# Optimization experiments

Measured on AMD Instinct MI355X. Metric: run time of the kernel, lower is better.

## Reference

```python
import jax, jax.numpy as jnp
import numpy as np

T_STEPS = 4000          # T_ms / dt = 1000 / 0.25
N_IN, N_OUT = 64, 10
HID = [1024, 1024]
DT, TAU = 0.25, 10.0
BETA = float(np.exp(-DT / TAU))   # beta_snn
THR = 1.0                          # thr_snn
SLOPE = 1.0                        # spike_snn uses slope=1.0
W_STD = 32.0                       # W_STD_CUBA

@jax.custom_vjp
def spike(u):
    # SurrogateSpike.forward: heaviside on (mem - thr)
    return (u >= 0).astype(u.dtype)

def _spike_fwd(u):
    return spike(u), u

def _spike_bwd(u, g):
    # fast-sigmoid surrogate: slope / (1 + slope*|u|)^2
    grad = SLOPE / (1.0 + SLOPE * jnp.abs(u)) ** 2
    return (g * grad,)

spike.defvjp(_spike_fwd, _spike_bwd)

def setup_inputs() -> dict:
    key = jax.random.key(0)
    ks = jax.random.split(key, 8)
    B = 16
    # Bernoulli(0.05) input spike train, time-major [T, B, N_IN]
    input_spikes = (jax.random.uniform(ks[0], (T_STEPS, B, N_IN)) < 0.05).astype(jnp.float32)
    sizes = [N_IN] + HID + [N_OUT]
    inp = {"input_spikes": input_spikes}
    for i, (n_pre, n_post) in enumerate(zip(sizes[:-1], sizes[1:])):
        # init_weight 'normal': clamp(N(0, W_STD), min=0) / n_pre
        w = jnp.maximum(jax.random.normal(ks[i + 1], (n_pre, n_post)) * W_STD, 0.0) / n_pre
        inp[f"W{i}"] = w.astype(jnp.float32)
        inp[f"b{i}"] = jnp.zeros((n_post,), jnp.float32)
    return inp

def reference(input_spikes, W0, b0, W1, b1, W2, b2):
    # Dale's law: feedforward weights clamped >= 0 in forward
    Ws = [jnp.maximum(W, 0.0) for W in (W0, W1, W2)]
    bs = [b0, b1, b2]
    B = input_spikes.shape[1]
    sizes = HID + [N_OUT]
    mems0 = tuple(jnp.zeros((B, n), input_spikes.dtype) for n in sizes)

    def step(mems, s_in):
        s = s_in
        new_mems = []
        for l in range(len(Ws)):
            I = s @ Ws[l] + bs[l]                 # [B, n_post]
            m = BETA * mems[l] + I                # LIF decay + drive
            sp = spike(m - THR)                   # surrogate-grad spike
            m = jnp.where(sp > 0, 0.0, m)         # hard reset to zero
            new_mems.append(m)
            s = sp
        return tuple(new_mems), s                 # emit output-layer spikes

    _, out_spikes = jax.lax.scan(step, mems0, input_spikes)
    return out_spikes  # [T, B, N_OUT]
```

## Files before the change

kernel.cpp:

```cpp
#include <hip/hip_runtime.h>
#include <hip/hip_bf16.h>
#include <math.h>


#define T_STEPS 4000
#define NB 16
#define N_IN 64
#define NH 1024
#define N_OUT 10
#define SEGO 40
#define SEGH 40

typedef __attribute__((ext_vector_type(8))) short bf16x8;
typedef __attribute__((ext_vector_type(4))) float f32x4;
typedef __hip_bfloat16 bf16;
typedef unsigned long long u64;

#define ASG(p) (const __attribute__((address_space(1))) void*)(p)
#define ASL(p) (__attribute__((address_space(3))) void*)(p)


__global__ __launch_bounds__(256) void k_prep(
    const float* __restrict__ in_sp, u64* __restrict__ mask,
    const float* __restrict__ W1, bf16* __restrict__ BT1,
    const float* __restrict__ W2, bf16* __restrict__ BT2,
    float* __restrict__ mst, int nM, int ZB, int MB) {
    __shared__ float Wlds[64][65];
    int b = blockIdx.x;
    const int tid = threadIdx.x;
    if (b < ZB) {
        int i = b * 256 + tid;
        if (i < nM) mst[i] = 0.f;
        return;
    }
    b -= ZB;
    if (b < MB) {
        int w = b * 4 + (tid >> 6);
        int lane = tid & 63;
        float v = in_sp[(size_t)w * 64 + lane];
        u64 bal = __ballot(v > 0.5f);
        if (lane == 0) mask[w] = bal;
        return;
    }
    b -= MB;
    if (b < 256) {
        const int lane = tid & 63;
        const int wr   = tid >> 6;
        const int k0 = (b & 15) * 64;
        const int n0 = (b >> 4) * 64;
#pragma unroll
        for (int rr = 0; rr < 16; ++rr) {
            int kl = wr * 16 + rr;
            Wlds[kl][lane] = W1[(size_t)(k0 + kl) * 1024 + n0 + lane];
        }
        __syncthreads();
#pragma unroll
        for (int rr = 0; rr < 16; ++rr) {
            int nl = wr * 16 + rr;
            float w = fmaxf(Wlds[lane][nl], 0.f);
            bf16 h = __float2bfloat16(w);
            float hf = __bfloat162float(h);
            bf16 l = __float2bfloat16(w - hf);
            size_t base = (size_t)(n0 + nl) * 2048 + 2 * k0 + lane;
            BT1[base] = h;
            BT1[base + 64] = l;
        }
        return;
    }
    b -= 256;
    {
        int idx = b * 256 + tid;
        int total = 128 * 2 * NH;
        if (idx >= total) return;
        int n  = idx / (2 * NH);
        int k2 = idx - n * (2 * NH);
        int lo = (k2 >= NH);
        int k = lo ? (k2 - NH) : k2;
        float v = 0.f;
        if (n < N_OUT) {
            float w = fmaxf(W2[(size_t)k * N_OUT + n], 0.f);
            float hi = __bfloat162float(__float2bfloat16(w));
            v = lo ? (w - hi) : w;
        }
        BT2[idx] = __float2bfloat16(v);
    }
}

__global__ void k_unpack(const u64* __restrict__ BITS, float* __restrict__ out,
                         int total) {
    int idx = blockIdx.x * 256 + threadIdx.x;
    if (idx >= total) return;
    int t   = idx / (NB * N_OUT);
    int rem = idx - t * (NB * N_OUT);
    int b = rem / N_OUT;
    int k = rem - b * N_OUT;
    u64 w = BITS[(size_t)(t / SEGO) * 256 + b * 16 + k];
    out[idx] = ((w >> (t % SEGO)) & 1ULL) ? 1.f : 0.f;
}


__device__ __forceinline__ void scan_out_body(
    const float* __restrict__ I2, const float* __restrict__ bias,
    float* __restrict__ mstate, u64* __restrict__ BITS,
    int Tc, float* seg, int tid) {
    float* segA = seg;
    float* segB = seg + SEGO * 256;
    const bool act = tid < 256;
    const int lane = tid & 63;
    const int wave = tid >> 6;
    const int k = tid & 15;
    float m = 0.f, bj = 0.f;
    if (act) {
        m = mstate[tid];
        bj = (k < N_OUT) ? bias[k] : 0.f;
    }
    const int nseg = Tc / SEGO;

#define O_PREFETCH(SEGBUF, SIDX)                                            \
    if (act) {                                                              \
        const float* src = I2 + (size_t)(SIDX) * SEGO * 256                 \
                              + (size_t)wave * 256 + lane * 4;              \
        _Pragma("unroll")                                                   \
        for (int g = 0; g < SEGO / 4; ++g)                                  \
            __builtin_amdgcn_global_load_lds(                               \
                ASG(src + (size_t)(g * 4) * 256),                           \
                ASL(&SEGBUF[(g * 4 + wave) * 256]), 16, 0, 0);              \
    }

#define O_PROC(SEGBUF, SIDX)                                                \
    if (act) {                                                              \
        u64 obits = 0;                                                      \
        _Pragma("unroll")                                                   \
        for (int sb = 0; sb < SEGO / 8; ++sb) {                             \
            float v[8];                                                     \
            _Pragma("unroll")                                               \
            for (int u = 0; u < 8; ++u)                                     \
                v[u] = SEGBUF[(sb * 8 + u) * 256 + tid];                    \
            _Pragma("unroll")                                               \
            for (int u = 0; u < 8; ++u) {                                   \
                m = fmaf(beta_c, m, v[u] + bj);                             \
                bool sp = (m >= 1.0f);                                      \
                obits |= ((u64)(sp ? 1 : 0)) << (sb * 8 + u);               \
                m = sp ? 0.f : m;                                           \
            }                                                               \
        }                                                                   \
        BITS[(size_t)(SIDX) * 256 + tid] = obits;                           \
    }

    const float beta_c = 0.97530991202833261687f;
    O_PREFETCH(segA, 0);
    O_PREFETCH(segB, 1);
    asm volatile("s_waitcnt vmcnt(10)" ::: "memory");
    __builtin_amdgcn_sched_barrier(0);
    __builtin_amdgcn_s_barrier();
    for (int s = 0; s < nseg; s += 2) {
        O_PROC(segA, s);
        if (s + 2 < nseg) {
            O_PREFETCH(segA, s + 2);
            asm volatile("s_waitcnt vmcnt(11)" ::: "memory");
        } else {
            asm volatile("s_waitcnt vmcnt(1)" ::: "memory");
        }
        __builtin_amdgcn_sched_barrier(0);
        __builtin_amdgcn_s_barrier();
        O_PROC(segB, s + 1);
        if (s + 3 < nseg) {
            O_PREFETCH(segB, s + 3);
            asm volatile("s_waitcnt vmcnt(11)" ::: "memory");
            __builtin_amdgcn_sched_barrier(0);
            __builtin_amdgcn_s_barrier();
        } else if (s + 2 < nseg) {
            asm volatile("s_waitcnt vmcnt(1)" ::: "memory");
            __builtin_amdgcn_sched_barrier(0);
            __builtin_amdgcn_s_barrier();
        }
    }
    if (act) mstate[tid] = m;
#undef O_PREFETCH
#undef O_PROC
}

__global__ __launch_bounds__(256) void k_scan_out(
    const float* __restrict__ I2, const float* __restrict__ bias,
    float* __restrict__ mstate, u64* __restrict__ BITS, int Tc) {
    __shared__ __align__(16) float seg[2 * SEGO * 256];
    scan_out_body(I2, bias, mstate, BITS, Tc, seg, threadIdx.x);
}


__global__ __launch_bounds__(256) void k_gemm_thin(
    const bf16* __restrict__ A, const bf16* __restrict__ BT,
    float* __restrict__ C) {
    const int tid  = threadIdx.x;
    const int lane = tid & 63;
    const int wave = tid >> 6;
    const int r16 = lane & 15;
    const int kg  = lane >> 4;
    const int m0 = blockIdx.x * 64 + wave * 16;
    f32x4 acc = {};
    const bf16* ap = A + (size_t)(m0 + r16) * 1024 + kg * 8;
    const bf16* bh = BT + (size_t)r16 * 2048 + kg * 8;
    const bf16* bl = bh + 1024;
#pragma unroll 8
    for (int kt = 0; kt < 32; ++kt) {
        const int ka = kt * 32;
        bf16x8 af  = *(const bf16x8*)(ap + ka);
        bf16x8 bfh = *(const bf16x8*)(bh + ka);
        bf16x8 bfl = *(const bf16x8*)(bl + ka);
        acc = __builtin_amdgcn_mfma_f32_16x16x32_bf16(af, bfh, acc, 0, 0, 0);
        acc = __builtin_amdgcn_mfma_f32_16x16x32_bf16(af, bfl, acc, 0, 0, 0);
    }
#pragma unroll
    for (int rr = 0; rr < 4; ++rr)
        C[(size_t)(m0 + kg * 4 + rr) * 16 + r16] = acc[rr];
}


__global__ __launch_bounds__(512) void k_gemm8(
    const bf16* __restrict__ A, const bf16* __restrict__ BT,
    float* __restrict__ C, int gx,
    const float* __restrict__ I2t, const float* __restrict__ b2t,
    float* __restrict__ m2t, u64* __restrict__ BITSt, int tcT, int doTail) {
    __shared__ __align__(16) char LDS[131072];
    const int tid  = threadIdx.x;

    if (doTail && (int)blockIdx.x == (int)gridDim.x - 1) {
        scan_out_body(I2t, b2t, m2t, BITSt, tcT, (float*)LDS, tid);
        return;
    }

    const int KA = 1024;
    const int nwg = gridDim.x - doTail;
    const int wg  = blockIdx.x;
    const int q = nwg >> 3, r = nwg & 7;
    const int xcd = wg & 7, idx0 = wg >> 3;
    const int swz = (xcd < r ? xcd * (q + 1) : r * (q + 1) + (xcd - r) * q) + idx0;
    const int gy = nwg / gx;
    const int n0 = (swz % gy) * 256;
    const int m0 = (swz / gy) * 256;

    const int lane = tid & 63;
    const int wave = tid >> 6;
    const int wm = (wave >> 2) * 128;
    const int wn = (wave & 3) * 64;
    const int r16l = lane & 15;
    const int kg   = lane >> 4;
    const int hA   = wave >> 2;
    const int hB   = (wave & 3) >> 1;
    const int wn64 = wave & 1;

    const int po = (r16l * 64 + kg * 16) ^ (((r16l >> 3) & 1) << 5);
    const char* bA[2] = { LDS + hA * 16384 + po,
                          LDS + 32768 + hA * 16384 + po };
    const char* bB[2] = { LDS + 65536 + hB * 16384 + po,
                          LDS + 98304 + hB * 16384 + po };
    const int bOff = wn64 * 8192;

    int s_row[2], s_col[2];
#pragma unroll
    for (int rr = 0; rr < 2; ++rr) {
        int d = (rr * 512 + tid) * 16;
        int l = d ^ (((d >> 9) & 1) << 5);
        int sub = l >> 10;
        int w = l & 1023;
        s_row[rr] = (sub >> 1) * 16 + (w >> 6);
        s_col[rr] = ((sub & 1) * 64 + (w & 63)) >> 1;
    }

#define STAGE_A(ADST, HALF, K0)                                             \
    {                                                                       \
        _Pragma("unroll")                                                   \
        for (int rr = 0; rr < 2; ++rr)                                      \
            __builtin_amdgcn_global_load_lds(                               \
                ASG(A + (size_t)(m0 + (HALF) * 128 + s_row[rr]) * KA        \
                    + (K0) + s_col[rr]),                                    \
                ASL(LDS + (ADST) * 32768 + (HALF) * 16384                   \
                    + (rr * 512 + wave * 64) * 16),                         \
                16, 0, 0);                                                  \
    }
#define STAGE_B(BUF, HALF, K0)                                              \
    {                                                                       \
        _Pragma("unroll")                                                   \
        for (int rr = 0; rr < 2; ++rr)                                      \
            __builtin_amdgcn_global_load_lds(                               \
                ASG(BT + (size_t)(n0 + (HALF) * 128 + s_row[rr]) * 2048     \
                    + (K0) + s_col[rr]),                                    \
                ASL(LDS + 65536 + (BUF) * 32768 + (HALF) * 16384            \
                    + (rr * 512 + wave * 64) * 16),                         \
                16, 0, 0);                                                  \
    }

    f32x4 acc[8][4] = {};
    bf16x8 a[4][2], b[4][2];

#define MM(MIB, NIB)                                                        \
    {                                                                       \
        _Pragma("unroll")                                                   \
        for (int i = 0; i < 4; ++i)                                         \
            _Pragma("unroll")                                               \
            for (int j = 0; j < 2; ++j) {                                   \
                acc[(MIB) + i][(NIB) + j] =                                 \
                    __builtin_amdgcn_mfma_f32_16x16x32_bf16(                \
                        a[i][0], b[(NIB) + j][0], acc[(MIB) + i][(NIB) + j], 0, 0, 0); \
                acc[(MIB) + i][(NIB) + j] =                                 \
                    __builtin_amdgcn_mfma_f32_16x16x32_bf16(                \
                        a[i][1], b[(NIB) + j][1], acc[(MIB) + i][(NIB) + j], 0, 0, 0); \
            }                                                               \
    }

#define PH_SYNC()                                                           \
    __builtin_amdgcn_s_barrier();                                           \
    asm volatile("s_waitcnt lgkmcnt(0)" ::: "memory");                      \
    __builtin_amdgcn_sched_barrier(0);

#define KT_EVEN(ABUF, BKN, AKN)                                             \
    {                                                                       \
        _Pragma("unroll")                                                   \
        for (int i = 0; i < 4; ++i) {                                       \
            a[i][0] = *(const bf16x8*)(bA[ABUF] + i * 2048);                \
            a[i][1] = *(const bf16x8*)(bA[ABUF] + i * 2048 + 1024);         \
        }                                                                   \
        _Pragma("unroll")                                                   \
        for (int j = 0; j < 2; ++j) {                                       \
            b[j][0] = *(const bf16x8*)(bB[0] + bOff + j * 2048);            \
            b[j][1] = *(const bf16x8*)(bB[0] + bOff + j * 2048 + 1024);     \
        }                                                                   \
        PH_SYNC();                                                          \
        __builtin_amdgcn_s_setprio(1);                                      \
        MM(0, 0);                                                           \
        __builtin_amdgcn_s_setprio(0);                                      \
        __builtin_amdgcn_s_barrier();                                       \
        _Pragma("unroll")                                                   \
        for (int j = 0; j < 2; ++j) {                                       \
            b[2 + j][0] = *(const bf16x8*)(bB[0] + bOff + (2 + j) * 2048);  \
            b[2 + j][1] = *(const bf16x8*)(bB[0] + bOff + (2 + j) * 2048 + 1024); \
        }                                                                   \
        PH_SYNC();                                                          \
        __builtin_amdgcn_s_setprio(1);                                      \
        MM(0, 2);                                                           \
        __builtin_amdgcn_s_setprio(0);                                      \
        __builtin_amdgcn_s_barrier();                                       \
        _Pragma("unroll")                                                   \
        for (int i = 0; i < 4; ++i) {                                       \
            a[i][0] = *(const bf16x8*)(bA[ABUF] + (4 + i) * 2048);          \
            a[i][1] = *(const bf16x8*)(bA[ABUF] + (4 + i) * 2048 + 1024);   \
        }                                                                   \
        STAGE_B(0, 0, BKN);                                                 \
        STAGE_B(0, 1, BKN);                                                 \
        PH_SYNC();                                                          \
        __builtin_amdgcn_s_setprio(1);                                      \
        MM(4, 0);                                                           \
        __builtin_amdgcn_s_setprio(0);                                      \
        __builtin_amdgcn_s_barrier();                                       \
        STAGE_A((ABUF) ^ 1, 0, AKN);                                        \
        STAGE_A((ABUF) ^ 1, 1, AKN);                                        \
        PH_SYNC();                                                          \
        __builtin_amdgcn_s_setprio(1);                                      \
        MM(4, 2);                                                           \
        __builtin_amdgcn_s_setprio(0);                                      \
        asm volatile("s_waitcnt vmcnt(8)" ::: "memory");                    \
        __builtin_amdgcn_sched_barrier(0);                                  \
        __builtin_amdgcn_s_barrier();                                       \
    }

#define KT_ODD(ABUF, BKN)                                                   \
    {                                                                       \
        _Pragma("unroll")                                                   \
        for (int i = 0; i < 4; ++i) {                                       \
            a[i][0] = *(const bf16x8*)(bA[ABUF] + i * 2048);                \
            a[i][1] = *(const bf16x8*)(bA[ABUF] + i * 2048 + 1024);         \
        }                                                                   \
        _Pragma("unroll")                                                   \
        for (int j = 0; j < 2; ++j) {                                       \
            b[j][0] = *(const bf16x8*)(bB[1] + bOff + j * 2048);            \
            b[j][1] = *(const bf16x8*)(bB[1] + bOff + j * 2048 + 1024);     \
        }                                                                   \
        PH_SYNC();                                                          \
        __builtin_amdgcn_s_setprio(1);                                      \
        MM(0, 0);                                                           \
        __builtin_amdgcn_s_setprio(0);                                      \
        __builtin_amdgcn_s_barrier();                                       \
        _Pragma("unroll")                                                   \
        for (int j = 0; j < 2; ++j) {                                       \
            b[2 + j][0] = *(const bf16x8*)(bB[1] + bOff + (2 + j) * 2048);  \
            b[2 + j][1] = *(const bf16x8*)(bB[1] + bOff + (2 + j) * 2048 + 1024); \
        }                                                                   \
        PH_SYNC();                                                          \
        __builtin_amdgcn_s_setprio(1);                                      \
        MM(0, 2);                                                           \
        __builtin_amdgcn_s_setprio(0);                                      \
        __builtin_amdgcn_s_barrier();                                       \
        _Pragma("unroll")                                                   \
        for (int i = 0; i < 4; ++i) {                                       \
            a[i][0] = *(const bf16x8*)(bA[ABUF] + (4 + i) * 2048);          \
            a[i][1] = *(const bf16x8*)(bA[ABUF] + (4 + i) * 2048 + 1024);   \
        }                                                                   \
        STAGE_B(1, 0, BKN);                                                 \
        STAGE_B(1, 1, BKN);                                                 \
        PH_SYNC();                                                          \
        __builtin_amdgcn_s_setprio(1);                                      \
        MM(4, 0);                                                           \
        __builtin_amdgcn_s_setprio(0);                                      \
        __builtin_amdgcn_s_barrier();                                       \
        PH_SYNC();                                                          \
        __builtin_amdgcn_s_setprio(1);                                      \
        MM(4, 2);                                                           \
        __builtin_amdgcn_s_setprio(0);                                      \
        asm volatile("s_waitcnt vmcnt(4)" ::: "memory");                    \
        __builtin_amdgcn_sched_barrier(0);                                  \
        __builtin_amdgcn_s_barrier();                                       \
    }

    STAGE_B(0, 0, 0);  STAGE_B(0, 1, 0);
    STAGE_A(0, 0, 0);  STAGE_A(0, 1, 0);
    STAGE_B(1, 0, 64); STAGE_B(1, 1, 64);
    asm volatile("s_waitcnt vmcnt(4)" ::: "memory");
    __builtin_amdgcn_sched_barrier(0);
    __builtin_amdgcn_s_barrier();

    for (int it2 = 0; it2 < 16; it2 += 2) {
        const int ak1 = (64 * (it2 + 1)) & 1023;
        const int be1 = (128 * (it2 + 1)) & 2047;
        KT_EVEN(0, be1, ak1);
        KT_ODD(0, be1 + 64);
        const int ak2 = (64 * (it2 + 2)) & 1023;
        const int be2 = (128 * (it2 + 2)) & 2047;
        KT_EVEN(1, be2, ak2);
        KT_ODD(1, be2 + 64);
    }
    asm volatile("s_waitcnt vmcnt(0)" ::: "memory");
    __builtin_amdgcn_sched_barrier(0);

#pragma unroll
    for (int mi = 0; mi < 8; ++mi)
#pragma unroll
        for (int ni = 0; ni < 4; ++ni)
#pragma unroll
            for (int rr = 0; rr < 4; ++rr) {
                int row = m0 + wm + mi * 16 + kg * 4 + rr;
                int col = n0 + wn + ni * 16 + r16l;
                C[(size_t)row * 1024 + col] = acc[mi][ni][rr];
            }
#undef KT_ODD
#undef KT_EVEN
#undef PH_SYNC
#undef MM
#undef STAGE_A
#undef STAGE_B
}


__global__ __launch_bounds__(64) void k_scan_l0(
    const u64* __restrict__ mask,
    const float* __restrict__ W0,
    const float* __restrict__ bias,
    float* __restrict__ mstate, bf16* __restrict__ S, int Tc, float beta) {
    __shared__ float Ilds[2][16][68];
    const int lane = threadIdx.x;
    const int gid  = blockIdx.x * 64 + lane;
    const int b  = blockIdx.x >> 4;
    const int q  = blockIdx.x & 15;
    const int j0 = q * 64;
    const int r16 = lane & 15;
    const int kg  = lane >> 4;
    bf16x8 bh[4][2], bl[4][2];
#pragma unroll
    for (int jt = 0; jt < 4; ++jt)
#pragma unroll
        for (int kk = 0; kk < 2; ++kk)
#pragma unroll
            for (int e = 0; e < 8; ++e) {
                int k = kk * 32 + kg * 8 + e;
                float w = fmaxf(W0[(size_t)k * 1024 + j0 + jt * 16 + r16], 0.f);
                bf16 h = __float2bfloat16(w);
                float hf = __bfloat162float(h);
                bf16 l = __float2bfloat16(w - hf);
                bh[jt][kk][e] = *(short*)&h;
                bl[jt][kk][e] = *(short*)&l;
            }
    float m = mstate[gid];
    const float bj = bias[j0 + lane];
    const size_t stride = (size_t)NB * NH;
    const int ntile = Tc / 16;
    const int tmax = ntile - 1;

#define LOADM(TT) mask[(size_t)(((TT) <= tmax ? (TT) : tmax) * 16 + r16) * NB + b]

#define L0_COMPUTE(MSK, P)                                                  \
    {                                                                       \
        f32x4 acc[4] = {};                                                  \
        _Pragma("unroll")                                                   \
        for (int kk = 0; kk < 2; ++kk) {                                    \
            unsigned byte8 = (unsigned)(((MSK) >> (kk * 32 + kg * 8)) & 0xFF); \
            bf16x8 af;                                                      \
            _Pragma("unroll")                                               \
            for (int e = 0; e < 8; ++e)                                     \
                af[e] = ((byte8 >> e) & 1) ? (short)0x3F80 : (short)0;      \
            _Pragma("unroll")                                               \
            for (int jt = 0; jt < 4; ++jt) {                                \
                acc[jt] = __builtin_amdgcn_mfma_f32_16x16x32_bf16(          \
                    af, bh[jt][kk], acc[jt], 0, 0, 0);                      \
                acc[jt] = __builtin_amdgcn_mfma_f32_16x16x32_bf16(          \
                    af, bl[jt][kk], acc[jt], 0, 0, 0);                      \
            }                                                               \
        }                                                                   \
        _Pragma("unroll")                                                   \
        for (int jt = 0; jt < 4; ++jt)                                      \
            _Pragma("unroll")                                               \
            for (int rr = 0; rr < 4; ++rr)                                  \
                Ilds[P][kg * 4 + rr][jt * 16 + r16] = acc[jt][rr];          \
    }

    u64 mc = LOADM(0);
    L0_COMPUTE(mc, 0);
    u64 mn = LOADM(1);
    for (int tt = 0; tt < ntile; ++tt) {
        __builtin_amdgcn_s_barrier();
        float v[16];
#pragma unroll
        for (int u = 0; u < 16; ++u)
            v[u] = Ilds[tt & 1][u][lane];
        u64 m2 = LOADM(tt + 2);
        if (tt + 1 < ntile) L0_COMPUTE(mn, (tt + 1) & 1);
        unsigned short o[16];
#pragma unroll
        for (int u = 0; u < 16; ++u) {
            m = fmaf(beta, m, v[u] + bj);
            bool sp = (m >= 1.0f);
            o[u] = sp ? (unsigned short)0x3F80 : (unsigned short)0;
            m = sp ? 0.f : m;
        }
#pragma unroll
        for (int u = 0; u < 16; ++u)
            ((unsigned short*)S)[(size_t)(tt * 16 + u) * stride + gid] = o[u];
        mn = m2;
    }
    mstate[gid] = m;
#undef L0_COMPUTE
#undef LOADM
}

__global__ __launch_bounds__(64) void k_scan_hidden(
    const float* __restrict__ I, const float* __restrict__ bias,
    float* __restrict__ mstate, bf16* __restrict__ S, int Tc, float beta) {
    __shared__ __align__(16) float segA[SEGH * 64];
    __shared__ __align__(16) float segB[SEGH * 64];
    const int lane = threadIdx.x;
    const int gid  = blockIdx.x * 64 + lane;
    const int j = gid & (NH - 1);
    float m = mstate[gid];
    const float bj = bias[j];
    const size_t stride = (size_t)NB * NH;
    const int nseg = Tc / SEGH;
    const int lrow = lane >> 4;
    const int lcol = (lane & 15) << 2;

#define H_PREFETCH(SEGBUF, SIDX)                                            \
    {                                                                       \
        const float* src = I + (size_t)(SIDX) * SEGH * stride               \
                             + (size_t)lrow * stride + blockIdx.x * 64 + lcol; \
        _Pragma("unroll")                                                   \
        for (int g = 0; g < SEGH / 4; ++g)                                  \
            __builtin_amdgcn_global_load_lds(                               \
                ASG(src + (size_t)(g * 4) * stride),                        \
                ASL(&SEGBUF[g * 256]), 16, 0, 0);                           \
    }

#define H_PROC(SEGBUF, SIDX)                                                \
    {                                                                       \
        const int btt = (SIDX) * SEGH;                                      \
        _Pragma("unroll")                                                   \
        for (int sb = 0; sb < SEGH / 8; ++sb) {                             \
            float v[8];                                                     \
            _Pragma("unroll")                                               \
            for (int u = 0; u < 8; ++u)                                     \
                v[u] = SEGBUF[(sb * 8 + u) * 64 + lane];                    \
            unsigned short o[8];                                            \
            _Pragma("unroll")                                               \
            for (int u = 0; u < 8; ++u) {                                   \
                m = fmaf(beta, m, v[u] + bj);                               \
                bool sp = (m >= 1.0f);                                      \
                o[u] = sp ? (unsigned short)0x3F80 : (unsigned short)0;     \
                m = sp ? 0.f : m;                                           \
            }                                                               \
            _Pragma("unroll")                                               \
            for (int u = 0; u < 8; ++u)                                     \
                ((unsigned short*)S)[(size_t)(btt + sb * 8 + u) * stride + gid] = o[u]; \
        }                                                                   \
    }

    H_PREFETCH(segA, 0);
    H_PREFETCH(segB, 1);
    asm volatile("s_waitcnt vmcnt(10)" ::: "memory");
    __builtin_amdgcn_sched_barrier(0);
    for (int s = 0; s < nseg; s += 2) {
        H_PROC(segA, s);
        if (s + 2 < nseg) {
            H_PREFETCH(segA, s + 2);
            asm volatile("s_waitcnt vmcnt(50)" ::: "memory");
        } else {
            asm volatile("s_waitcnt vmcnt(40)" ::: "memory");
        }
        __builtin_amdgcn_sched_barrier(0);
        H_PROC(segB, s + 1);
        if (s + 3 < nseg) {
            H_PREFETCH(segB, s + 3);
            asm volatile("s_waitcnt vmcnt(50)" ::: "memory");
            __builtin_amdgcn_sched_barrier(0);
        } else if (s + 2 < nseg) {
            asm volatile("s_waitcnt vmcnt(40)" ::: "memory");
            __builtin_amdgcn_sched_barrier(0);
        }
    }
    mstate[gid] = m;
#undef H_PREFETCH
#undef H_PROC
}


extern "C" void kernel_launch(void* const* d_in, const int* in_sizes, int n_in,
                              void* d_out, int out_size, void* d_ws, size_t ws_size,
                              hipStream_t stream) {
    const float* in_sp = (const float*)d_in[0];
    const float* W0 = (const float*)d_in[1];
    const float* b0 = (const float*)d_in[2];
    const float* W1 = (const float*)d_in[3];
    const float* b1 = (const float*)d_in[4];
    const float* W2 = (const float*)d_in[5];
    const float* b2 = (const float*)d_in[6];
    float* out = (float*)d_out;

    char* p = (char*)d_ws;
    auto carve = [&](size_t bytes) -> void* {
        char* r = p; p += (bytes + 255) & ~(size_t)255; return (void*)r;
    };
    u64*  MASK  = (u64*)carve((size_t)T_STEPS * NB * 8);
    bf16* BT1   = (bf16*)carve((size_t)NH * 2 * NH * 2);
    bf16* BT2   = (bf16*)carve((size_t)128 * 2 * NH * 2);
    float* m0s  = (float*)carve((size_t)NB * NH * 4);
    float* m1s  = (float*)carve((size_t)NB * NH * 4);
    float* m2s  = (float*)carve((size_t)NB * 16 * 4);
    float* I2BUF = (float*)carve((size_t)T_STEPS * NB * 16 * 4);
    u64*  BITS  = (u64*)carve((size_t)(T_STEPS / SEGO) * 256 * 8);
    size_t fixed = (size_t)(p - (char*)d_ws);

    const int tc_opts[3] = {2000, 800, 400};
    int Tc = 400;
    for (int i = 0; i < 3; ++i) {
        size_t Mc_ = (size_t)tc_opts[i] * NB;
        size_t need = fixed
            + ((Mc_ * NH * 4 + 255) & ~(size_t)255)
            + ((Mc_ * NH * 2 + 255) & ~(size_t)255);
        if (need <= ws_size) { Tc = tc_opts[i]; break; }
    }
    size_t Mc = (size_t)Tc * NB;
    float* IBUF = (float*)carve(Mc * NH * 4);
    bf16*  S    = (bf16*)carve(Mc * NH * 2);

    const float beta = (float)exp(-0.25 / 10.0);

    int nM = NB * NH * 2 + NB * 16;
    const int ZB = (nM + 255) / 256;
    const int MB = (T_STEPS * NB) / 4;
    const int L2B = (128 * 2 * NH + 255) / 256;
    k_prep<<<ZB + MB + 256 + L2B, 256, 0, stream>>>(
        in_sp, MASK, W1, BT1, W2, BT2, m0s, nM, ZB, MB);

    const int C = T_STEPS / Tc;
    const int gx8 = (int)(Mc / 256);
    const int gthin = (int)(Mc / 64);
    for (int c = 0; c < C; ++c) {
        int t0 = c * Tc;
        k_scan_l0<<<256, 64, 0, stream>>>(MASK + (size_t)t0 * NB, W0, b0,
                                          m0s, S, Tc, beta);
        if (c == 0) {
            k_gemm8<<<gx8 * 4, 512, 0, stream>>>(S, BT1, IBUF, gx8,
                                                 nullptr, nullptr, nullptr,
                                                 nullptr, 0, 0);
        } else {
            int tp = (c - 1) * Tc;
            k_gemm8<<<gx8 * 4 + 1, 512, 0, stream>>>(
                S, BT1, IBUF, gx8,
                I2BUF + (size_t)tp * NB * 16, b2, m2s,
                BITS + (size_t)(tp / SEGO) * 256, Tc, 1);
        }
        k_scan_hidden<<<(NB * NH) / 64, 64, 0, stream>>>(IBUF, b1, m1s, S, Tc, beta);
        k_gemm_thin<<<gthin, 256, 0, stream>>>(S, BT2,
                                               I2BUF + (size_t)t0 * NB * 16);
    }
    int tl = (C - 1) * Tc;
    k_scan_out<<<1, 256, 0, stream>>>(I2BUF + (size_t)tl * NB * 16, b2, m2s,
                                      BITS + (size_t)(tl / SEGO) * 256, Tc);
    int nOut = T_STEPS * NB * N_OUT;
    k_unpack<<<(nOut + 255) / 256, 256, 0, stream>>>(BITS, out, nOut);
}
```

Baseline: 658.5 us.

## Overlap next chunk's layer-0 scan with current GEMM via double-buffered spikes

Layer-0 scan work for chunk c+1 is folded into the k_gemm8 launch as 32 extra workgroups of 8 waves each, writing into a second spike buffer. This lets the serial layer-0 scan run alongside the big hidden-layer GEMM instead of as its own launch. The cost is extra workspace for the double buffer, with a fallback to separate launches when it does not fit. Each extra workgroup's waves share one CU, and those workgroups may delay GEMM tiles.

```diff
diff --git a/kernel.cpp b/kernel.cpp
--- a/kernel.cpp
+++ b/kernel.cpp
@@ -18,6 +18,8 @@
 
 #define ASG(p) (const __attribute__((address_space(1))) void*)(p)
 #define ASL(p) (__attribute__((address_space(3))) void*)(p)
+
+#define BETA_C 0.97530991202833261687f
 
 
 __global__ __launch_bounds__(256) void k_prep(
@@ -138,7 +140,7 @@
                 v[u] = SEGBUF[(sb * 8 + u) * 256 + tid];                    \
             _Pragma("unroll")                                               \
             for (int u = 0; u < 8; ++u) {                                   \
-                m = fmaf(beta_c, m, v[u] + bj);                             \
+                m = fmaf(BETA_C, m, v[u] + bj);                             \
                 bool sp = (m >= 1.0f);                                      \
                 obits |= ((u64)(sp ? 1 : 0)) << (sb * 8 + u);               \
                 m = sp ? 0.f : m;                                           \
@@ -147,7 +149,6 @@
         BITS[(size_t)(SIDX) * 256 + tid] = obits;                           \
     }
 
-    const float beta_c = 0.97530991202833261687f;
     O_PREFETCH(segA, 0);
     O_PREFETCH(segB, 1);
     asm volatile("s_waitcnt vmcnt(10)" ::: "memory");
@@ -185,6 +186,102 @@
     float* __restrict__ mstate, u64* __restrict__ BITS, int Tc) {
     __shared__ __align__(16) float seg[2 * SEGO * 256];
     scan_out_body(I2, bias, mstate, BITS, Tc, seg, threadIdx.x);
+}
+
+
+__device__ __forceinline__ void scan_l0_body(
+    const u64* __restrict__ mask, const float* __restrict__ W0,
+    const float* __restrict__ bias, float* __restrict__ mstate,
+    bf16* __restrict__ S, int Tc, int b0, int lane, float* IL) {
+    const int b  = b0 >> 4;
+    const int q  = b0 & 15;
+    const int j0 = q * 64;
+    const int gid = b0 * 64 + lane;
+    const int r16 = lane & 15;
+    const int kg  = lane >> 4;
+    bf16x8 bh[4][2], bl[4][2];
+#pragma unroll
+    for (int jt = 0; jt < 4; ++jt)
+#pragma unroll
+        for (int kk = 0; kk < 2; ++kk)
+#pragma unroll
+            for (int e = 0; e < 8; ++e) {
+                int k = kk * 32 + kg * 8 + e;
+                float w = fmaxf(W0[(size_t)k * 1024 + j0 + jt * 16 + r16], 0.f);
+                bf16 h = __float2bfloat16(w);
+                float hf = __bfloat162float(h);
+                bf16 l = __float2bfloat16(w - hf);
+                bh[jt][kk][e] = *(short*)&h;
+                bl[jt][kk][e] = *(short*)&l;
+            }
+    float m = mstate[gid];
+    const float bj = bias[j0 + lane];
+    const size_t stride = (size_t)NB * NH;
+    const int ntile = Tc / 16;
+    const int tmax = ntile - 1;
+
+#define LOADM(TT) mask[(size_t)(((TT) <= tmax ? (TT) : tmax) * 16 + r16) * NB + b]
+
+#define L0_COMPUTE(MSK, P)                                                  \
+    {                                                                       \
+        f32x4 acc[4] = {};                                                  \
+        _Pragma("unroll")                                                   \
+        for (int kk = 0; kk < 2; ++kk) {                                    \
+            unsigned byte8 = (unsigned)(((MSK) >> (kk * 32 + kg * 8)) & 0xFF); \
+            bf16x8 af;                                                      \
+            _Pragma("unroll")                                               \
+            for (int e = 0; e < 8; ++e)                                     \
+                af[e] = ((byte8 >> e) & 1) ? (short)0x3F80 : (short)0;      \
+            _Pragma("unroll")                                               \
+            for (int jt = 0; jt < 4; ++jt) {                                \
+                acc[jt] = __builtin_amdgcn_mfma_f32_16x16x32_bf16(          \
+                    af, bh[jt][kk], acc[jt], 0, 0, 0);                      \
+                acc[jt] = __builtin_amdgcn_mfma_f32_16x16x32_bf16(          \
+                    af, bl[jt][kk], acc[jt], 0, 0, 0);                      \
+            }                                                               \
+        }                                                                   \
+        _Pragma("unroll")                                                   \
+        for (int jt = 0; jt < 4; ++jt)                                      \
+            _Pragma("unroll")                                               \
+            for (int rr = 0; rr < 4; ++rr)                                  \
+                IL[(P) * 1088 + (kg * 4 + rr) * 68 + jt * 16 + r16] = acc[jt][rr]; \
+    }
+
+    u64 mc = LOADM(0);
+    L0_COMPUTE(mc, 0);
+    u64 mn = LOADM(1);
+    for (int tt = 0; tt < ntile; ++tt) {
+        __builtin_amdgcn_s_barrier();
+        float v[16];
+#pragma unroll
+        for (int u = 0; u < 16; ++u)
+            v[u] = IL[(tt & 1) * 1088 + u * 68 + lane];
+        u64 m2 = LOADM(tt + 2);
+        if (tt + 1 < ntile) L0_COMPUTE(mn, (tt + 1) & 1);
+        unsigned short o[16];
+#pragma unroll
+        for (int u = 0; u < 16; ++u) {
+            m = fmaf(BETA_C, m, v[u] + bj);
+            bool sp = (m >= 1.0f);
+            o[u] = sp ? (unsigned short)0x3F80 : (unsigned short)0;
+            m = sp ? 0.f : m;
+        }
+#pragma unroll
+        for (int u = 0; u < 16; ++u)
+            ((unsigned short*)S)[(size_t)(tt * 16 + u) * stride + gid] = o[u];
+        mn = m2;
+    }
+    mstate[gid] = m;
+#undef L0_COMPUTE
+#undef LOADM
+}
+
+__global__ __launch_bounds__(64) void k_scan_l0(
+    const u64* __restrict__ mask, const float* __restrict__ W0,
+    const float* __restrict__ bias, float* __restrict__ mstate,
+    bf16* __restrict__ S, int Tc) {
+    __shared__ __align__(16) float IL[2 * 16 * 68];
+    scan_l0_body(mask, W0, bias, mstate, S, Tc, blockIdx.x, threadIdx.x, IL);
 }
 
 
@@ -220,18 +317,30 @@
     const bf16* __restrict__ A, const bf16* __restrict__ BT,
     float* __restrict__ C, int gx,
     const float* __restrict__ I2t, const float* __restrict__ b2t,
-    float* __restrict__ m2t, u64* __restrict__ BITSt, int tcT, int doTail) {
+    float* __restrict__ m2t, u64* __restrict__ BITSt, int tcT, int doTailOut,
+    const u64* __restrict__ maskN, const float* __restrict__ W0N,
+    const float* __restrict__ b0N, float* __restrict__ m0N,
+    bf16* __restrict__ SN, int nL0blk) {
     __shared__ __align__(16) char LDS[131072];
     const int tid  = threadIdx.x;
-
-    if (doTail && (int)blockIdx.x == (int)gridDim.x - 1) {
-        scan_out_body(I2t, b2t, m2t, BITSt, tcT, (float*)LDS, tid);
+    const int lane = tid & 63;
+    const int wave = tid >> 6;
+
+    const int nwg = gridDim.x - doTailOut - nL0blk;
+    const int wg  = blockIdx.x;
+    if (wg >= nwg) {
+        int tix = wg - nwg;
+        if (tix < doTailOut) {
+            scan_out_body(I2t, b2t, m2t, BITSt, tcT, (float*)LDS, tid);
+        } else {
+            int unit = (tix - doTailOut) * 8 + wave;
+            float* IL = (float*)LDS + wave * 2176;
+            scan_l0_body(maskN, W0N, b0N, m0N, SN, tcT, unit, lane, IL);
+        }
         return;
     }
 
     const int KA = 1024;
-    const int nwg = gridDim.x - doTail;
-    const int wg  = blockIdx.x;
     const int q = nwg >> 3, r = nwg & 7;
     const int xcd = wg & 7, idx0 = wg >> 3;
     const int swz = (xcd < r ? xcd * (q + 1) : r * (q + 1) + (xcd - r) * q) + idx0;
@@ -239,8 +348,6 @@
     const int n0 = (swz % gy) * 256;
     const int m0 = (swz / gy) * 256;
 
-    const int lane = tid & 63;
-    const int wave = tid >> 6;
     const int wm = (wave >> 2) * 128;
     const int wn = (wave & 3) * 64;
     const int r16l = lane & 15;
@@ -450,96 +557,6 @@
 }
 
 
-__global__ __launch_bounds__(64) void k_scan_l0(
-    const u64* __restrict__ mask,
-    const float* __restrict__ W0,
-    const float* __restrict__ bias,
-    float* __restrict__ mstate, bf16* __restrict__ S, int Tc, float beta) {
-    __shared__ float Ilds[2][16][68];
-    const int lane = threadIdx.x;
-    const int gid  = blockIdx.x * 64 + lane;
-    const int b  = blockIdx.x >> 4;
-    const int q  = blockIdx.x & 15;
-    const int j0 = q * 64;
-    const int r16 = lane & 15;
-    const int kg  = lane >> 4;
-    bf16x8 bh[4][2], bl[4][2];
-#pragma unroll
-    for (int jt = 0; jt < 4; ++jt)
-#pragma unroll
-        for (int kk = 0; kk < 2; ++kk)
-#pragma unroll
-            for (int e = 0; e < 8; ++e) {
-                int k = kk * 32 + kg * 8 + e;
-                float w = fmaxf(W0[(size_t)k * 1024 + j0 + jt * 16 + r16], 0.f);
-                bf16 h = __float2bfloat16(w);
-                float hf = __bfloat162float(h);
-                bf16 l = __float2bfloat16(w - hf);
-                bh[jt][kk][e] = *(short*)&h;
-                bl[jt][kk][e] = *(short*)&l;
-            }
-    float m = mstate[gid];
-    const float bj = bias[j0 + lane];
-    const size_t stride = (size_t)NB * NH;
-    const int ntile = Tc / 16;
-    const int tmax = ntile - 1;
-
-#define LOADM(TT) mask[(size_t)(((TT) <= tmax ? (TT) : tmax) * 16 + r16) * NB + b]
-
-#define L0_COMPUTE(MSK, P)                                                  \
-    {                                                                       \
-        f32x4 acc[4] = {};                                                  \
-        _Pragma("unroll")                                                   \
-        for (int kk = 0; kk < 2; ++kk) {                                    \
-            unsigned byte8 = (unsigned)(((MSK) >> (kk * 32 + kg * 8)) & 0xFF); \
-            bf16x8 af;                                                      \
-            _Pragma("unroll")                                               \
-            for (int e = 0; e < 8; ++e)                                     \
-                af[e] = ((byte8 >> e) & 1) ? (short)0x3F80 : (short)0;      \
-            _Pragma("unroll")                                               \
-            for (int jt = 0; jt < 4; ++jt) {                                \
-                acc[jt] = __builtin_amdgcn_mfma_f32_16x16x32_bf16(          \
-                    af, bh[jt][kk], acc[jt], 0, 0, 0);                      \
-                acc[jt] = __builtin_amdgcn_mfma_f32_16x16x32_bf16(          \
-                    af, bl[jt][kk], acc[jt], 0, 0, 0);                      \
-            }                                                               \
-        }                                                                   \
-        _Pragma("unroll")                                                   \
-        for (int jt = 0; jt < 4; ++jt)                                      \
-            _Pragma("unroll")                                               \
-            for (int rr = 0; rr < 4; ++rr)                                  \
-                Ilds[P][kg * 4 + rr][jt * 16 + r16] = acc[jt][rr];          \
-    }
-
-    u64 mc = LOADM(0);
-    L0_COMPUTE(mc, 0);
-    u64 mn = LOADM(1);
-    for (int tt = 0; tt < ntile; ++tt) {
-        __builtin_amdgcn_s_barrier();
-        float v[16];
-#pragma unroll
-        for (int u = 0; u < 16; ++u)
-            v[u] = Ilds[tt & 1][u][lane];
-        u64 m2 = LOADM(tt + 2);
-        if (tt + 1 < ntile) L0_COMPUTE(mn, (tt + 1) & 1);
-        unsigned short o[16];
-#pragma unroll
-        for (int u = 0; u < 16; ++u) {
-            m = fmaf(beta, m, v[u] + bj);
-            bool sp = (m >= 1.0f);
-            o[u] = sp ? (unsigned short)0x3F80 : (unsigned short)0;
-            m = sp ? 0.f : m;
-        }
-#pragma unroll
-        for (int u = 0; u < 16; ++u)
-            ((unsigned short*)S)[(size_t)(tt * 16 + u) * stride + gid] = o[u];
-        mn = m2;
-    }
-    mstate[gid] = m;
-#undef L0_COMPUTE
-#undef LOADM
-}
-
 __global__ __launch_bounds__(64) void k_scan_hidden(
     const float* __restrict__ I, const float* __restrict__ bias,
     float* __restrict__ mstate, bf16* __restrict__ S, int Tc, float beta) {
@@ -655,9 +672,11 @@
     }
     size_t Mc = (size_t)Tc * NB;
     float* IBUF = (float*)carve(Mc * NH * 4);
-    bf16*  S    = (bf16*)carve(Mc * NH * 2);
-
-    const float beta = (float)exp(-0.25 / 10.0);
+    bf16*  S0   = (bf16*)carve(Mc * NH * 2);
+    size_t sbytes = (Mc * NH * 2 + 255) & ~(size_t)255;
+    int sdbuf = ((size_t)(p - (char*)d_ws) + sbytes <= ws_size) ? 1 : 0;
+    bf16* S1 = sdbuf ? (bf16*)carve(Mc * NH * 2) : S0;
+    auto Sb = [&](int c) -> bf16* { return (c & 1) ? S1 : S0; };
 
     int nM = NB * NH * 2 + NB * 16;
     const int ZB = (nM + 255) / 256;
@@ -669,24 +688,27 @@
     const int C = T_STEPS / Tc;
     const int gx8 = (int)(Mc / 256);
     const int gthin = (int)(Mc / 64);
+
+    k_scan_l0<<<256, 64, 0, stream>>>(MASK, W0, b0, m0s, Sb(0), Tc);
+
+    const float beta = (float)exp(-0.25 / 10.0);
     for (int c = 0; c < C; ++c) {
         int t0 = c * Tc;
-        k_scan_l0<<<256, 64, 0, stream>>>(MASK + (size_t)t0 * NB, W0, b0,
-                                          m0s, S, Tc, beta);
-        if (c == 0) {
-            k_gemm8<<<gx8 * 4, 512, 0, stream>>>(S, BT1, IBUF, gx8,
-                                                 nullptr, nullptr, nullptr,
-                                                 nullptr, 0, 0);
-        } else {
-            int tp = (c - 1) * Tc;
-            k_gemm8<<<gx8 * 4 + 1, 512, 0, stream>>>(
-                S, BT1, IBUF, gx8,
-                I2BUF + (size_t)tp * NB * 16, b2, m2s,
-                BITS + (size_t)(tp / SEGO) * 256, Tc, 1);
-        }
-        k_scan_hidden<<<(NB * NH) / 64, 64, 0, stream>>>(IBUF, b1, m1s, S, Tc, beta);
-        k_gemm_thin<<<gthin, 256, 0, stream>>>(S, BT2,
+        int doOut = (c >= 1) ? 1 : 0;
+        int nL0   = (sdbuf && c + 1 < C) ? 32 : 0;
+        int tp = (c - 1) * Tc;
+        k_gemm8<<<gx8 * 4 + doOut + nL0, 512, 0, stream>>>(
+            Sb(c), BT1, IBUF, gx8,
+            doOut ? I2BUF + (size_t)tp * NB * 16 : nullptr, b2, m2s,
+            doOut ? BITS + (size_t)(tp / SEGO) * 256 : nullptr, Tc, doOut,
+            nL0 ? MASK + (size_t)(t0 + Tc) * NB : nullptr, W0, b0, m0s,
+            nL0 ? Sb(c + 1) : nullptr, nL0);
+        k_scan_hidden<<<(NB * NH) / 64, 64, 0, stream>>>(IBUF, b1, m1s, Sb(c), Tc, beta);
+        k_gemm_thin<<<gthin, 256, 0, stream>>>(Sb(c), BT2,
                                                I2BUF + (size_t)t0 * NB * 16);
+        if (!sdbuf && c + 1 < C)
+            k_scan_l0<<<256, 64, 0, stream>>>(MASK + (size_t)(t0 + Tc) * NB,
+                                              W0, b0, m0s, Sb(c + 1), Tc);
     }
     int tl = (C - 1) * Tc;
     k_scan_out<<<1, 256, 0, stream>>>(I2BUF + (size_t)tl * NB * 16, b2, m2s,
```

Result: no change. 657.9 us, median of 2 (-0.1%).
